# Performance work log

Measured on AMD Instinct MI355X. Metric: run time of the kernel, lower is better.

The kernel has to match this reference:

```python
import jax, jax.numpy as jnp
import numpy as np

HID = 256
IN_LSTM = 512
LAYER_NUM = 2


def _lstm_step(x, h, c, Wih, Whh, bih, bhh):
    # PyTorch LSTMCell: gates = x@Wih.T + bih + h@Whh.T + bhh, order i,f,g,o
    g = x @ Wih.T + bih + h @ Whh.T + bhh
    i, f, gg, o = jnp.split(g, 4, axis=-1)
    i = jax.nn.sigmoid(i); f = jax.nn.sigmoid(f)
    gg = jnp.tanh(gg); o = jax.nn.sigmoid(o)
    c2 = f * c + i * gg
    return o * jnp.tanh(c2), c2


def _run_direction(seq, Wih, Whh, bih, bhh, w_time, ts):
    # seq: [T, B, 512]; merge h/c via time_w_layer every ts steps;
    # at the merge step the *merged* h is written to the output buffer.
    T, B, _ = seq.shape
    chunks = seq.reshape(T // ts, ts, B, IN_LSTM)

    def chunk_fn(carry, xc):  # xc: [ts, B, 512]
        def step(hc, xt):
            h2, c2 = _lstm_step(xt, hc[0], hc[1], Wih, Whh, bih, bhh)
            return (h2, c2), (h2, c2)
        _, (hs, cs) = jax.lax.scan(step, carry, xc)  # hs: [ts, B, 256]
        hm = jnp.einsum('tbd,t->bd', hs, w_time)
        cm = jnp.einsum('tbd,t->bd', cs, w_time)
        return (hm, cm), hs.at[-1].set(hm)

    h0 = jnp.zeros((B, HID), seq.dtype)
    _, outs = jax.lax.scan(chunk_fn, (h0, h0), chunks)  # [T//ts, ts, B, 256]
    return outs.reshape(T, B, HID)


def setup_inputs() -> dict:
    key = jax.random.key(0)
    ks = jax.random.split(key, 16)
    B, T, D_IN, D_OUT, TS = 128, 1024, 128, 8, 8
    s_in = 1.0 / np.sqrt(D_IN)
    s_l = 1.0 / np.sqrt(HID)
    s_o = 1.0 / np.sqrt(2 * HID)
    return {
        'x': jax.random.normal(ks[0], (B, T, D_IN), jnp.float32),
        'W_in': jax.random.uniform(ks[1], (IN_LSTM, D_IN), jnp.float32, -s_in, s_in),
        'b_in': jax.random.uniform(ks[2], (IN_LSTM,), jnp.float32, -s_in, s_in),
        'Wih1': jax.random.uniform(ks[3], (4 * HID, IN_LSTM), jnp.float32, -s_l, s_l),
        'Whh1': jax.random.uniform(ks[4], (4 * HID, HID), jnp.float32, -s_l, s_l),
        'bih1': jax.random.uniform(ks[5], (4 * HID,), jnp.float32, -s_l, s_l),
        'bhh1': jax.random.uniform(ks[6], (4 * HID,), jnp.float32, -s_l, s_l),
        'Wih2': jax.random.uniform(ks[7], (4 * HID, IN_LSTM), jnp.float32, -s_l, s_l),
        'Whh2': jax.random.uniform(ks[8], (4 * HID, HID), jnp.float32, -s_l, s_l),
        'bih2': jax.random.uniform(ks[9], (4 * HID,), jnp.float32, -s_l, s_l),
        'bhh2': jax.random.uniform(ks[10], (4 * HID,), jnp.float32, -s_l, s_l),
        'w_time1': jax.random.uniform(ks[11], (TS,), jnp.float32, -1.0 / np.sqrt(TS), 1.0 / np.sqrt(TS)),
        'w_time2': jax.random.uniform(ks[12], (TS,), jnp.float32, -1.0 / np.sqrt(TS), 1.0 / np.sqrt(TS)),
        'W_out': jax.random.uniform(ks[13], (D_OUT, 2 * HID), jnp.float32, -s_o, s_o),
        'b_out': jax.random.uniform(ks[14], (D_OUT,), jnp.float32, -s_o, s_o),
        'batch_size': B,
        'time_steps': TS,
        'length': T,
        'r': 1,
    }


def reference(x, W_in, b_in, Wih1, Whh1, bih1, bhh1, Wih2, Whh2, bih2, bhh2,
              w_time1, w_time2, W_out, b_out, batch_size, time_steps, length, r):
    ts = int(time_steps)
    out = x @ W_in.T + b_in  # [B, T, 512]; dropout is identity in eval
    for _ in range(LAYER_NUM):
        seq = jnp.transpose(out, (1, 0, 2))  # [T, B, 512]
        o1 = _run_direction(seq, Wih1, Whh1, bih1, bhh1, w_time1, ts)
        # backward direction processes reversed input; outputs are stored in
        # processing order (NOT re-reversed), matching the original code.
        o2 = _run_direction(seq[::-1], Wih2, Whh2, bih2, bhh2, w_time2, ts)
        out = jnp.transpose(jnp.concatenate([o1, o2], axis=-1), (1, 0, 2))  # [B, T, 512]
    out = out @ W_out.T + b_out  # [B, T, output_dim]
    return jax.nn.log_softmax(out, axis=1)  # LogSoftmax(dim=1) over time, as in source
```

## Files before the change

### kernel.cpp

```cpp
#include <hip/hip_runtime.h>
#include <stdint.h>
#include <stddef.h>

#define HIDN 256
#define GATES 1024
#define INL 512
#define BB 128
#define TT 1024
#define TSS 8
#define DIN 128
#define DOUT 8

typedef unsigned short u16;
typedef unsigned int u32;
typedef unsigned long long u64;
typedef __bf16 bf16x8_t __attribute__((ext_vector_type(8)));
typedef float f32x4_t __attribute__((ext_vector_type(4)));
typedef short s16x8_t __attribute__((ext_vector_type(8)));
typedef u16 u16x4_t __attribute__((ext_vector_type(4)));

union V8 { s16x8_t s; bf16x8_t b; };
union U64x2 { u64 q[2]; s16x8_t s; };

#define MRK 0x0001000100010001ull

__device__ __forceinline__ u16 f2bf(float f){
  unsigned u = __builtin_bit_cast(unsigned, f);
  u += 0x7FFFu + ((u >> 16) & 1u);
  return (u16)(u >> 16);
}
__device__ __forceinline__ float bf2f(u16 h){
  unsigned u = ((unsigned)h) << 16;
  return __builtin_bit_cast(float, u);
}
__device__ __forceinline__ float sigmoidf_(float x){ return 1.f/(1.f + __expf(-x)); }
__device__ __forceinline__ float tanhf_(float x){
  float ax = fabsf(x);
  float e = __expf(-2.f*ax);
  float t = (1.f - e)/(1.f + e);
  return x < 0.f ? -t : t;
}

__global__ __launch_bounds__(256) void cvt_f32_bf16(const float* __restrict__ in,
                                                    u16* __restrict__ out, int n4){
  int i = blockIdx.x*256 + threadIdx.x;
  if (i < n4){
    float4 f = ((const float4*)in)[i];
    u16x4_t u;
    u[0] = f2bf(f.x); u[1] = f2bf(f.y); u[2] = f2bf(f.z); u[3] = f2bf(f.w);
    ((u16x4_t*)out)[i] = u;
  }
}

__global__ __launch_bounds__(256) void pack_whh(const float* __restrict__ Whh,
                                                u16* __restrict__ wf){
  int idx = blockIdx.x*256 + threadIdx.x;
  int l  = idx & 63;
  int kt = (idx >> 6) & 7;
  int nt = idx >> 9;
  int j = nt*16 + (l & 15);
  int k = kt*32 + (l >> 4)*8;
  const float* src = Whh + (long)j*HIDN + k;
  s16x8_t pk;
  #pragma unroll
  for (int e=0;e<8;e++) pk[e] = (short)f2bf(src[e]);
  *(s16x8_t*)(wf + (long)idx*8) = pk;
}

template<int XA, int OM>
__global__ __launch_bounds__(256, 2) void gemm_tile(
    const void* __restrict__ Av, const u16* __restrict__ W,
    u16* __restrict__ C,
    const float* __restrict__ bias1, const float* __restrict__ bias2,
    int K, int N, int srcT0, int sdir)
{
  __shared__ u16 As[128*32];
  __shared__ u16 Ws[128*32];
  const int tid = threadIdx.x;
  const int l = tid & 63, wid = tid >> 6;
  const int lr = l & 15, lg = l >> 4;
  const int wm = (wid >> 1)*64, wn = (wid & 1)*64;
  const int by = blockIdx.y, bx = blockIdx.x;
  const int n0 = bx*128;
  const int m0 = by*128;

  f32x4_t acc[4][4];
  #pragma unroll
  for (int i=0;i<4;i++)
    #pragma unroll
    for (int j=0;j<4;j++){ f32x4_t z = {0.f,0.f,0.f,0.f}; acc[i][j] = z; }

  const long abase = (long)(srcT0 + sdir*by)*128;
  const int srow = l >> 2;
  const int scol = (l & 3)*8;

  for (int k0 = 0; k0 < K; k0 += 32){
    __syncthreads();
    if (XA == 0){
      const u16* A = (const u16*)Av;
      #pragma unroll
      for (int c=0;c<2;c++){
        const int rb = wid*16 + c*64;
        __builtin_amdgcn_global_load_lds(
          (const __attribute__((address_space(1))) void*)
              (A + (abase + rb + srow)*(long)K + k0 + scol),
          (__attribute__((address_space(3))) void*)(&As[rb*32]),
          16, 0, 0);
      }
    } else {
      const float* A = (const float*)Av;
      const int xT = srcT0 + sdir*by;
      const int r0 = tid >> 2, c0 = (tid & 3)*8;
      #pragma unroll
      for (int c=0;c<2;c++){
        int row = r0 + c*64;
        const float* src = A + ((long)row*1024 + xT)*128 + k0 + c0;
        float4 f0 = *(const float4*)src;
        float4 f1 = *(const float4*)(src + 4);
        s16x8_t pk;
        pk[0]=(short)f2bf(f0.x); pk[1]=(short)f2bf(f0.y);
        pk[2]=(short)f2bf(f0.z); pk[3]=(short)f2bf(f0.w);
        pk[4]=(short)f2bf(f1.x); pk[5]=(short)f2bf(f1.y);
        pk[6]=(short)f2bf(f1.z); pk[7]=(short)f2bf(f1.w);
        *(s16x8_t*)(&As[row*32 + c0]) = pk;
      }
    }
    #pragma unroll
    for (int c=0;c<2;c++){
      const int rb = wid*16 + c*64;
      __builtin_amdgcn_global_load_lds(
        (const __attribute__((address_space(1))) void*)
            (W + (long)(n0 + rb + srow)*K + k0 + scol),
        (__attribute__((address_space(3))) void*)(&Ws[rb*32]),
        16, 0, 0);
    }
    __syncthreads();

    V8 af[4], bfr[4];
    #pragma unroll
    for (int i=0;i<4;i++)
      af[i].s = *(const s16x8_t*)(&As[(wm + i*16 + lr)*32 + lg*8]);
    #pragma unroll
    for (int j=0;j<4;j++)
      bfr[j].s = *(const s16x8_t*)(&Ws[(wn + j*16 + lr)*32 + lg*8]);
    #pragma unroll
    for (int i=0;i<4;i++)
      #pragma unroll
      for (int j=0;j<4;j++)
        acc[i][j] = __builtin_amdgcn_mfma_f32_16x16x32_bf16(af[i].b, bfr[j].b, acc[i][j], 0,0,0);
  }

  #pragma unroll
  for (int i=0;i<4;i++){
    #pragma unroll
    for (int j=0;j<4;j++){
      if (OM == 0){
        int col = n0 + wn + j*16 + lr;
        float bb = bias1 ? bias1[col] : 0.f;
        if (bias2) bb += bias2[col];
        #pragma unroll
        for (int r=0;r<4;r++){
          int mrow = m0 + wm + i*16 + lg*4 + r;
          C[(long)mrow*N + col] = f2bf(acc[i][j][r] + bb);
        }
      } else {
        int colb = n0 + wn + j*16;
        int col = colb + lr;
        int g   = colb >> 8;
        int hb2 = (colb >> 7) & 1;
        int w2  = (colb >> 4) & 7;
        int slice = (wm >> 4) + i;
        float bb = bias1[col] + bias2[col];
        u16x4_t v;
        #pragma unroll
        for (int r=0;r<4;r++) v[r] = f2bf(acc[i][j][r] + bb);
        long dst = ((((long)by*8 + slice)*2 + hb2)*8 + w2)*1024
                 + (long)l*16 + g*4;
        *(u16x4_t*)(C + dst) = v;
      }
    }
  }
}

__global__ __launch_bounds__(512, 2) void lstm_rec7(
    const u16* __restrict__ pre0, const u16* __restrict__ pre1,
    const u16* __restrict__ wf0, const u16* __restrict__ wf1,
    const float* __restrict__ wt0, const float* __restrict__ wt1,
    u16* __restrict__ out,
    int outBase, int CT, int isFirst,
    u16* __restrict__ hstate,
    float* __restrict__ cstate,
    u16* __restrict__ hx)
{
  const int bid = blockIdx.x;
  const int hb  = bid >> 4;
  const int p   = bid & 15;
  const int dir = p >> 3, slice = p & 7;
  const int tid = threadIdx.x;
  const int l = tid & 63, w = tid >> 6;
  const int lr = l & 15, lg = l >> 4;

  const u16*   wf  = dir ? wf1 : wf0;
  const float* wtg = dir ? wt1 : wt0;
  const u16*   pre = dir ? pre1 : pre0;

  V8 bwOwn[4][4], bwPeer[4][4];
  #pragma unroll
  for (int g=0; g<4; g++){
    const int nt = g*16 + hb*8 + w;
    const u16* base = wf + ((long)nt*8*64 + l)*8;
    const long ownOff  = (long)(hb*4)*64*8;
    const long peerOff = (long)((1-hb)*4)*64*8;
    #pragma unroll
    for (int j=0; j<4; j++){
      bwOwn [g][j].s = *(const s16x8_t*)(base + ownOff  + (long)j*64*8);
      bwPeer[g][j].s = *(const s16x8_t*)(base + peerOff + (long)j*64*8);
    }
  }

  __shared__ u16 h_buf[2][16][136];

  const int cr = tid >> 5, cc4 = (tid & 31)*4;
  u64 h0v = 0;
  if (!isFirst){
    const u16* src = hstate + dir*32768 + (slice*16 + cr)*256 + hb*128 + cc4;
    h0v = *(const u64*)src;
  }
  *(u64*)&h_buf[0][cr][cc4] = h0v;
  float c[4], hacc[4] = {0,0,0,0}, cacc[4] = {0,0,0,0};
  {
    const long cb = ((long)(dir*16 + slice*2 + hb)*512 + tid)*4;
    #pragma unroll
    for (int r=0;r<4;r++) c[r] = isFirst ? 0.f : cstate[cb + r];
  }
  float wreg[8];
  #pragma unroll
  for (int i=0;i<8;i++) wreg[i] = wtg[i];

  u16*       myx   = hx + (long)(p*2 + hb)*2*2048;
  const u16* peerx = hx + (long)(p*2 + (1-hb))*2*2048;

  __hip_atomic_store((u64*)(myx + cr*128 + cc4), h0v & ~MRK,
                     __ATOMIC_RELAXED, __HIP_MEMORY_SCOPE_AGENT);
  __syncthreads();

  const u16* preT = pre + (((long)slice*2 + hb)*8 + w)*1024 + (long)l*16;
  s16x8_t pfA = *(const s16x8_t*)(preT);
  s16x8_t pfB = *(const s16x8_t*)(preT + 8);

  for (int t = 0; t < CT; t++){
    f32x4_t acc[4];
    #pragma unroll
    for (int r=0; r<4; r++){
      acc[0][r] = bf2f((u16)pfA[r]);
      acc[1][r] = bf2f((u16)pfA[4+r]);
      acc[2][r] = bf2f((u16)pfB[r]);
      acc[3][r] = bf2f((u16)pfB[4+r]);
    }
    if (t + 1 < CT){
      const u16* pp = preT + (long)(t+1)*131072;
      pfA = *(const s16x8_t*)(pp);
      pfB = *(const s16x8_t*)(pp + 8);
    }

    const u64 exp = ((t>>1)&1) ? MRK : 0ull;
    const u64* qb = (const u64*)(peerx + (long)(t&1)*2048)
                  + (lr*32 + lg*2);
    u64 q[8];
    #pragma unroll
    for (int j=0;j<4;j++)
      #pragma unroll
      for (int k=0;k<2;k++)
        q[j*2+k] = __hip_atomic_load(qb + j*8 + k,
                      __ATOMIC_RELAXED, __HIP_MEMORY_SCOPE_AGENT);

    {
      V8 af[4];
      const u16* hb0 = &h_buf[t&1][lr][lg*8];
      #pragma unroll
      for (int j=0;j<4;j++)
        af[j].s = *(const s16x8_t*)(hb0 + j*32);
      #pragma unroll
      for (int g=0;g<4;g++)
        #pragma unroll
        for (int j=0;j<4;j++)
          acc[g] = __builtin_amdgcn_mfma_f32_16x16x32_bf16(
              af[j].b, bwOwn[g][j].b, acc[g], 0,0,0);
    }

    {
      int tries = 0;
      while (true){
        int ok = 1;
        #pragma unroll
        for (int i=0;i<8;i++) ok &= ((q[i] & MRK) == exp);
        if (__all(ok)) break;
        if (++tries > (1<<16)) break;
        __builtin_amdgcn_s_sleep(1);
        #pragma unroll
        for (int j=0;j<4;j++)
          #pragma unroll
          for (int k=0;k<2;k++)
            q[j*2+k] = __hip_atomic_load(qb + j*8 + k,
                          __ATOMIC_RELAXED, __HIP_MEMORY_SCOPE_AGENT);
      }
    }
    {
      V8 pafr[4];
      #pragma unroll
      for (int j=0;j<4;j++){
        U64x2 uq;
        uq.q[0] = q[j*2]; uq.q[1] = q[j*2+1];
        pafr[j].s = uq.s;
      }
      #pragma unroll
      for (int g=0;g<4;g++)
        #pragma unroll
        for (int j=0;j<4;j++)
          acc[g] = __builtin_amdgcn_mfma_f32_16x16x32_bf16(
              pafr[j].b, bwPeer[g][j].b, acc[g], 0,0,0);
    }

    const float wtv = wreg[t & 7];
    const bool last = (t & 7) == 7;
    float hout[4];
    #pragma unroll
    for (int r=0;r<4;r++){
      float iv = sigmoidf_(acc[0][r]);
      float fv = sigmoidf_(acc[1][r]);
      float gv = tanhf_  (acc[2][r]);
      float ov = sigmoidf_(acc[3][r]);
      float cn = fv*c[r] + iv*gv;
      float hh = ov*tanhf_(cn);
      float ha = hacc[r] + wtv*hh;
      float ca = cacc[r] + wtv*cn;
      hout[r] = last ? ha : hh;
      c[r]    = last ? ca : cn;
      hacc[r] = last ? 0.f : ha;
      cacc[r] = last ? 0.f : ca;
    }

    #pragma unroll
    for (int r=0;r<4;r++)
      h_buf[(t+1)&1][lg*4 + r][w*16 + lr] = f2bf(hout[r]);
    __syncthreads();

    if (t < CT - 1){
      const u64 pm = (((t+1)>>1)&1) ? MRK : 0ull;
      u64 v = *(const u64*)&h_buf[(t+1)&1][cr][cc4];
      v = (v & ~MRK) | pm;
      __hip_atomic_store((u64*)(myx + (long)((t+1)&1)*2048 + cr*128 + cc4), v,
                         __ATOMIC_RELAXED, __HIP_MEMORY_SCOPE_AGENT);
    }

    {
      u16x4_t v = *(const u16x4_t*)&h_buf[(t+1)&1][cr][cc4];
      const long orow = (long)(outBase + t)*128 + slice*16 + cr;
      *(u16x4_t*)(out + orow*512 + dir*256 + hb*128 + cc4) = v;
    }
  }

  {
    u16* dst = hstate + dir*32768 + (slice*16 + cr)*256 + hb*128 + cc4;
    *(u16x4_t*)dst = *(const u16x4_t*)&h_buf[CT&1][cr][cc4];
  }
  {
    const long cb = ((long)(dir*16 + slice*2 + hb)*512 + tid)*4;
    #pragma unroll
    for (int r=0;r<4;r++) cstate[cb + r] = c[r];
  }
}

__global__ __launch_bounds__(256) void kout(const u16* __restrict__ Ab,
    const u16* __restrict__ Wo, const float* __restrict__ bo,
    float* __restrict__ op, int chunkRow0)
{
  __shared__ u16 Ws[4096];
  __shared__ u16 Rs[32*520];
  const int tid = threadIdx.x;
  {
    int f = tid*8;
    *(s16x8_t*)&Ws[f] = *(const s16x8_t*)(Wo + f);
    *(s16x8_t*)&Ws[f+2048] = *(const s16x8_t*)(Wo + f + 2048);
  }
  const long row0 = (long)blockIdx.x*32;
  #pragma unroll
  for (int i=0;i<8;i++){
    int f = tid*8 + i*2048;
    int rr = f >> 9, cc = f & 511;
    *(s16x8_t*)&Rs[rr*520 + cc] = *(const s16x8_t*)(Ab + (row0+rr)*512 + cc);
  }
  __syncthreads();
  const int rr = tid >> 3, d = tid & 7;
  float s = bo[d];
  for (int k=0;k<512;k+=8){
    s16x8_t a = *(const s16x8_t*)&Rs[rr*520 + k];
    s16x8_t wv = *(const s16x8_t*)&Ws[d*512 + k];
    #pragma unroll
    for (int e=0;e<8;e++)
      s += bf2f((u16)a[e]) * bf2f((u16)wv[e]);
  }
  const long grow = chunkRow0 + row0 + rr;
  const int tt = (int)(grow >> 7), b2 = (int)(grow & 127);
  op[((long)b2*1024 + tt)*8 + d] = s;
}

__global__ __launch_bounds__(256) void lsm(float* __restrict__ io){
  const int b = blockIdx.x >> 3, d = blockIdx.x & 7;
  const int tid = threadIdx.x;
  __shared__ float red[4];
  float v[4];
  float mx = -3.4e38f;
  const long base = (long)b*1024*8 + d;
  #pragma unroll
  for (int i=0;i<4;i++){
    v[i] = io[base + (long)(tid + i*256)*8];
    mx = fmaxf(mx, v[i]);
  }
  #pragma unroll
  for (int off=32; off>=1; off>>=1) mx = fmaxf(mx, __shfl_down(mx, off, 64));
  if ((tid & 63) == 0) red[tid >> 6] = mx;
  __syncthreads();
  mx = fmaxf(fmaxf(red[0],red[1]), fmaxf(red[2],red[3]));
  __syncthreads();
  float s = 0.f;
  #pragma unroll
  for (int i=0;i<4;i++) s += __expf(v[i]-mx);
  #pragma unroll
  for (int off=32; off>=1; off>>=1) s += __shfl_down(s, off, 64);
  if ((tid & 63) == 0) red[tid >> 6] = s;
  __syncthreads();
  s = red[0]+red[1]+red[2]+red[3];
  float lse = mx + __logf(s);
  #pragma unroll
  for (int i=0;i<4;i++) io[base + (long)(tid + i*256)*8] = v[i] - lse;
}

extern "C" void kernel_launch(void* const* d_in, const int* in_sizes, int n_in,
                              void* d_out, int out_size, void* d_ws, size_t ws_size,
                              hipStream_t stream){
  const float* x     = (const float*)d_in[0];
  const float* W_in  = (const float*)d_in[1];
  const float* b_in  = (const float*)d_in[2];
  const float* Wih1  = (const float*)d_in[3];
  const float* Whh1  = (const float*)d_in[4];
  const float* bih1  = (const float*)d_in[5];
  const float* bhh1  = (const float*)d_in[6];
  const float* Wih2  = (const float*)d_in[7];
  const float* Whh2  = (const float*)d_in[8];
  const float* bih2  = (const float*)d_in[9];
  const float* bhh2  = (const float*)d_in[10];
  const float* wt1   = (const float*)d_in[11];
  const float* wt2   = (const float*)d_in[12];
  const float* W_out = (const float*)d_in[13];
  const float* b_out = (const float*)d_in[14];

  auto rnd = [](size_t b){ return (b + 255) & ~(size_t)255; };

  const size_t ACT1B   = (size_t)TT*BB*512*2;
  const size_t WIHB    = (size_t)GATES*INL*2;
  const size_t WFRAGB  = (size_t)GATES*HIDN*2;
  const size_t WINB    = (size_t)INL*DIN*2;
  const size_t WOUTB   = (size_t)DOUT*INL*2;
  const size_t HSTB    = (size_t)2*BB*HIDN*2;
  const size_t CSTB    = (size_t)32*512*4*4;
  const size_t HXB     = (size_t)32*2*2048*2;

  const size_t fixedB = rnd(ACT1B) + 2*rnd(WIHB) + 2*rnd(WFRAGB) + rnd(WINB)
                      + rnd(WOUTB) + rnd(HSTB) + rnd(CSTB) + rnd(HXB);

  int CT = 8;
  const int cands[8] = {1024,512,256,128,64,32,16,8};
  for (int ci = 0; ci < 8; ci++){
    int cand = cands[ci];
    size_t need = fixedB + rnd((size_t)cand*BB*512*2) + 2*rnd((size_t)cand*BB*GATES*2);
    if (need <= ws_size){ CT = cand; break; }
  }
  const int nc = TT / CT;

  char* ws = (char*)d_ws;
  size_t off = 0;
  auto alloc = [&](size_t bytes) -> void* {
    void* p = ws + off;
    off += rnd(bytes);
    return p;
  };

  u16*   act1    = (u16*)alloc(ACT1B);
  u16*   Wihb0   = (u16*)alloc(WIHB);
  u16*   Wihb1   = (u16*)alloc(WIHB);
  u16*   wfrag0  = (u16*)alloc(WFRAGB);
  u16*   wfrag1  = (u16*)alloc(WFRAGB);
  u16*   Winb    = (u16*)alloc(WINB);
  u16*   Woutb   = (u16*)alloc(WOUTB);
  u16*   hstate  = (u16*)alloc(HSTB);
  float* cstate  = (float*)alloc(CSTB);
  u16*   hx      = (u16*)alloc(HXB);
  u16*   actchunk= (u16*)alloc((size_t)CT*BB*512*2);
  u16*   pre0    = (u16*)alloc((size_t)CT*BB*GATES*2);
  u16*   pre1    = (u16*)alloc((size_t)CT*BB*GATES*2);

  hipMemsetAsync(hx, 0xFF, HXB, stream);

  cvt_f32_bf16<<<(GATES*INL/4 + 255)/256, 256, 0, stream>>>(Wih1, Wihb0, GATES*INL/4);
  cvt_f32_bf16<<<(GATES*INL/4 + 255)/256, 256, 0, stream>>>(Wih2, Wihb1, GATES*INL/4);
  cvt_f32_bf16<<<(INL*DIN/4 + 255)/256, 256, 0, stream>>>(W_in, Winb, INL*DIN/4);
  cvt_f32_bf16<<<(DOUT*INL/4 + 255)/256, 256, 0, stream>>>(W_out, Woutb, DOUT*INL/4);
  pack_whh<<<128, 256, 0, stream>>>(Whh1, wfrag0);
  pack_whh<<<128, 256, 0, stream>>>(Whh2, wfrag1);

  for (int c2 = 0; c2 < nc; c2++){
    gemm_tile<1,0><<<dim3(4, CT), 256, 0, stream>>>(x, Winb, actchunk,
        b_in, nullptr, DIN, 512, c2*CT, 1);
    gemm_tile<0,1><<<dim3(8, CT), 256, 0, stream>>>(actchunk, Wihb0, pre0,
        bih1, bhh1, INL, GATES, 0, 1);
    gemm_tile<1,0><<<dim3(4, CT), 256, 0, stream>>>(x, Winb, actchunk,
        b_in, nullptr, DIN, 512, 1023 - c2*CT, -1);
    gemm_tile<0,1><<<dim3(8, CT), 256, 0, stream>>>(actchunk, Wihb1, pre1,
        bih2, bhh2, INL, GATES, 0, 1);
    lstm_rec7<<<dim3(32), 512, 0, stream>>>(pre0, pre1, wfrag0, wfrag1,
        wt1, wt2, act1, c2*CT, CT, c2 == 0, hstate, cstate, hx);
  }

  for (int c2 = 0; c2 < nc; c2++){
    gemm_tile<0,1><<<dim3(8, CT), 256, 0, stream>>>(act1, Wihb0, pre0,
        bih1, bhh1, INL, GATES, c2*CT, 1);
    gemm_tile<0,1><<<dim3(8, CT), 256, 0, stream>>>(act1, Wihb1, pre1,
        bih2, bhh2, INL, GATES, 1023 - c2*CT, -1);
    lstm_rec7<<<dim3(32), 512, 0, stream>>>(pre0, pre1, wfrag0, wfrag1,
        wt1, wt2, actchunk, 0, CT, c2 == 0, hstate, cstate, hx);
    kout<<<CT*4, 256, 0, stream>>>(actchunk, Woutb, b_out,
        (float*)d_out, c2*CT*128);
  }

  lsm<<<BB*DOUT, 256, 0, stream>>>((float*)d_out);
}
```

Baseline: 8.580 ms.

## Merge paired LSTM recurrence blocks into one 1024-thread block, dropping cross-block spin sync

Each recurrence block previously covered half the hidden units and swapped h halves with its partner through global-memory atomics and spin-waits at every timestep. Now one 1024-thread block per (direction, batch slice) holds all 256 hidden units, keeps the full Whh fragment set in registers, and reads the whole h from shared memory, so per-step sync is just __syncthreads. The precomputed-gate layout is changed to match, and the hx exchange buffer and its memset are removed. The cost is half as many blocks (16) and twice the register weight load per thread, which could limit occupancy or cause spills.

After: 22.09 ms. 157% more time.

```diff
diff --git a/kernel.cpp b/kernel.cpp
--- a/kernel.cpp
+++ b/kernel.cpp
@@ -20,9 +20,6 @@
 typedef u16 u16x4_t __attribute__((ext_vector_type(4)));
 
 union V8 { s16x8_t s; bf16x8_t b; };
-union U64x2 { u64 q[2]; s16x8_t s; };
-
-#define MRK 0x0001000100010001ull
 
 __device__ __forceinline__ u16 f2bf(float f){
   unsigned u = __builtin_bit_cast(unsigned, f);
@@ -167,34 +164,30 @@
         int colb = n0 + wn + j*16;
         int col = colb + lr;
         int g   = colb >> 8;
-        int hb2 = (colb >> 7) & 1;
-        int w2  = (colb >> 4) & 7;
+        int w2  = (colb >> 4) & 15;
         int slice = (wm >> 4) + i;
         float bb = bias1[col] + bias2[col];
         u16x4_t v;
         #pragma unroll
         for (int r=0;r<4;r++) v[r] = f2bf(acc[i][j][r] + bb);
-        long dst = ((((long)by*8 + slice)*2 + hb2)*8 + w2)*1024
-                 + (long)l*16 + g*4;
+        long dst = (((long)by*8 + slice)*16 + w2)*1024
+                 + (long)(lg*16 + lr)*16 + g*4;
         *(u16x4_t*)(C + dst) = v;
       }
     }
   }
 }
 
-__global__ __launch_bounds__(512, 2) void lstm_rec7(
+__global__ __launch_bounds__(1024, 4) void lstm_rec9(
     const u16* __restrict__ pre0, const u16* __restrict__ pre1,
     const u16* __restrict__ wf0, const u16* __restrict__ wf1,
     const float* __restrict__ wt0, const float* __restrict__ wt1,
     u16* __restrict__ out,
     int outBase, int CT, int isFirst,
     u16* __restrict__ hstate,
-    float* __restrict__ cstate,
-    u16* __restrict__ hx)
+    float* __restrict__ cstate)
 {
-  const int bid = blockIdx.x;
-  const int hb  = bid >> 4;
-  const int p   = bid & 15;
+  const int p = blockIdx.x;
   const int dir = p >> 3, slice = p & 7;
   const int tid = threadIdx.x;
   const int l = tid & 63, w = tid >> 6;
@@ -204,32 +197,27 @@
   const float* wtg = dir ? wt1 : wt0;
   const u16*   pre = dir ? pre1 : pre0;
 
-  V8 bwOwn[4][4], bwPeer[4][4];
+  V8 bw[4][8];
   #pragma unroll
   for (int g=0; g<4; g++){
-    const int nt = g*16 + hb*8 + w;
+    const int nt = g*16 + w;
     const u16* base = wf + ((long)nt*8*64 + l)*8;
-    const long ownOff  = (long)(hb*4)*64*8;
-    const long peerOff = (long)((1-hb)*4)*64*8;
-    #pragma unroll
-    for (int j=0; j<4; j++){
-      bwOwn [g][j].s = *(const s16x8_t*)(base + ownOff  + (long)j*64*8);
-      bwPeer[g][j].s = *(const s16x8_t*)(base + peerOff + (long)j*64*8);
-    }
-  }
-
-  __shared__ u16 h_buf[2][16][136];
-
-  const int cr = tid >> 5, cc4 = (tid & 31)*4;
+    #pragma unroll
+    for (int kt=0; kt<8; kt++)
+      bw[g][kt].s = *(const s16x8_t*)(base + (long)kt*64*8);
+  }
+
+  __shared__ u16 h_buf[2][16][264];
+
+  const int cr = tid >> 6, cc4 = (tid & 63)*4;
   u64 h0v = 0;
-  if (!isFirst){
-    const u16* src = hstate + dir*32768 + (slice*16 + cr)*256 + hb*128 + cc4;
-    h0v = *(const u64*)src;
-  }
+  if (!isFirst)
+    h0v = *(const u64*)(hstate + dir*32768 + (slice*16 + cr)*256 + cc4);
   *(u64*)&h_buf[0][cr][cc4] = h0v;
+
   float c[4], hacc[4] = {0,0,0,0}, cacc[4] = {0,0,0,0};
   {
-    const long cb = ((long)(dir*16 + slice*2 + hb)*512 + tid)*4;
+    const long cb = ((long)p*1024 + tid)*4;
     #pragma unroll
     for (int r=0;r<4;r++) c[r] = isFirst ? 0.f : cstate[cb + r];
   }
@@ -237,14 +225,9 @@
   #pragma unroll
   for (int i=0;i<8;i++) wreg[i] = wtg[i];
 
-  u16*       myx   = hx + (long)(p*2 + hb)*2*2048;
-  const u16* peerx = hx + (long)(p*2 + (1-hb))*2*2048;
-
-  __hip_atomic_store((u64*)(myx + cr*128 + cc4), h0v & ~MRK,
-                     __ATOMIC_RELAXED, __HIP_MEMORY_SCOPE_AGENT);
   __syncthreads();
 
-  const u16* preT = pre + (((long)slice*2 + hb)*8 + w)*1024 + (long)l*16;
+  const u16* preT = pre + ((long)slice*16 + w)*1024 + (long)l*16;
   s16x8_t pfA = *(const s16x8_t*)(preT);
   s16x8_t pfB = *(const s16x8_t*)(preT + 8);
 
@@ -263,62 +246,14 @@
       pfB = *(const s16x8_t*)(pp + 8);
     }
 
-    const u64 exp = ((t>>1)&1) ? MRK : 0ull;
-    const u64* qb = (const u64*)(peerx + (long)(t&1)*2048)
-                  + (lr*32 + lg*2);
-    u64 q[8];
-    #pragma unroll
-    for (int j=0;j<4;j++)
+    #pragma unroll
+    for (int kt=0; kt<8; kt++){
+      V8 af;
+      af.s = *(const s16x8_t*)(&h_buf[t&1][lr][kt*32 + lg*8]);
       #pragma unroll
-      for (int k=0;k<2;k++)
-        q[j*2+k] = __hip_atomic_load(qb + j*8 + k,
-                      __ATOMIC_RELAXED, __HIP_MEMORY_SCOPE_AGENT);
-
-    {
-      V8 af[4];
-      const u16* hb0 = &h_buf[t&1][lr][lg*8];
-      #pragma unroll
-      for (int j=0;j<4;j++)
-        af[j].s = *(const s16x8_t*)(hb0 + j*32);
-      #pragma unroll
-      for (int g=0;g<4;g++)
-        #pragma unroll
-        for (int j=0;j<4;j++)
-          acc[g] = __builtin_amdgcn_mfma_f32_16x16x32_bf16(
-              af[j].b, bwOwn[g][j].b, acc[g], 0,0,0);
-    }
-
-    {
-      int tries = 0;
-      while (true){
-        int ok = 1;
-        #pragma unroll
-        for (int i=0;i<8;i++) ok &= ((q[i] & MRK) == exp);
-        if (__all(ok)) break;
-        if (++tries > (1<<16)) break;
-        __builtin_amdgcn_s_sleep(1);
-        #pragma unroll
-        for (int j=0;j<4;j++)
-          #pragma unroll
-          for (int k=0;k<2;k++)
-            q[j*2+k] = __hip_atomic_load(qb + j*8 + k,
-                          __ATOMIC_RELAXED, __HIP_MEMORY_SCOPE_AGENT);
-      }
-    }
-    {
-      V8 pafr[4];
-      #pragma unroll
-      for (int j=0;j<4;j++){
-        U64x2 uq;
-        uq.q[0] = q[j*2]; uq.q[1] = q[j*2+1];
-        pafr[j].s = uq.s;
-      }
-      #pragma unroll
-      for (int g=0;g<4;g++)
-        #pragma unroll
-        for (int j=0;j<4;j++)
-          acc[g] = __builtin_amdgcn_mfma_f32_16x16x32_bf16(
-              pafr[j].b, bwPeer[g][j].b, acc[g], 0,0,0);
+      for (int g=0; g<4; g++)
+        acc[g] = __builtin_amdgcn_mfma_f32_16x16x32_bf16(
+            af.b, bw[g][kt].b, acc[g], 0,0,0);
     }
 
     const float wtv = wreg[t & 7];
@@ -345,27 +280,17 @@
       h_buf[(t+1)&1][lg*4 + r][w*16 + lr] = f2bf(hout[r]);
     __syncthreads();
 
-    if (t < CT - 1){
-      const u64 pm = (((t+1)>>1)&1) ? MRK : 0ull;
+    {
       u64 v = *(const u64*)&h_buf[(t+1)&1][cr][cc4];
-      v = (v & ~MRK) | pm;
-      __hip_atomic_store((u64*)(myx + (long)((t+1)&1)*2048 + cr*128 + cc4), v,
-                         __ATOMIC_RELAXED, __HIP_MEMORY_SCOPE_AGENT);
-    }
-
-    {
-      u16x4_t v = *(const u16x4_t*)&h_buf[(t+1)&1][cr][cc4];
       const long orow = (long)(outBase + t)*128 + slice*16 + cr;
-      *(u16x4_t*)(out + orow*512 + dir*256 + hb*128 + cc4) = v;
-    }
-  }
-
+      *(u64*)(out + orow*512 + dir*256 + cc4) = v;
+    }
+  }
+
+  *(u64*)(hstate + dir*32768 + (slice*16 + cr)*256 + cc4)
+      = *(const u64*)&h_buf[CT&1][cr][cc4];
   {
-    u16* dst = hstate + dir*32768 + (slice*16 + cr)*256 + hb*128 + cc4;
-    *(u16x4_t*)dst = *(const u16x4_t*)&h_buf[CT&1][cr][cc4];
-  }
-  {
-    const long cb = ((long)(dir*16 + slice*2 + hb)*512 + tid)*4;
+    const long cb = ((long)p*1024 + tid)*4;
     #pragma unroll
     for (int r=0;r<4;r++) cstate[cb + r] = c[r];
   }
@@ -463,11 +388,10 @@
   const size_t WINB    = (size_t)INL*DIN*2;
   const size_t WOUTB   = (size_t)DOUT*INL*2;
   const size_t HSTB    = (size_t)2*BB*HIDN*2;
-  const size_t CSTB    = (size_t)32*512*4*4;
-  const size_t HXB     = (size_t)32*2*2048*2;
+  const size_t CSTB    = (size_t)16*1024*4*4;
 
   const size_t fixedB = rnd(ACT1B) + 2*rnd(WIHB) + 2*rnd(WFRAGB) + rnd(WINB)
-                      + rnd(WOUTB) + rnd(HSTB) + rnd(CSTB) + rnd(HXB);
+                      + rnd(WOUTB) + rnd(HSTB) + rnd(CSTB);
 
   int CT = 8;
   const int cands[8] = {1024,512,256,128,64,32,16,8};
@@ -495,12 +419,9 @@
   u16*   Woutb   = (u16*)alloc(WOUTB);
   u16*   hstate  = (u16*)alloc(HSTB);
   float* cstate  = (float*)alloc(CSTB);
-  u16*   hx      = (u16*)alloc(HXB);
   u16*   actchunk= (u16*)alloc((size_t)CT*BB*512*2);
   u16*   pre0    = (u16*)alloc((size_t)CT*BB*GATES*2);
   u16*   pre1    = (u16*)alloc((size_t)CT*BB*GATES*2);
-
-  hipMemsetAsync(hx, 0xFF, HXB, stream);
 
   cvt_f32_bf16<<<(GATES*INL/4 + 255)/256, 256, 0, stream>>>(Wih1, Wihb0, GATES*INL/4);
   cvt_f32_bf16<<<(GATES*INL/4 + 255)/256, 256, 0, stream>>>(Wih2, Wihb1, GATES*INL/4);
@@ -518,8 +439,8 @@
         b_in, nullptr, DIN, 512, 1023 - c2*CT, -1);
     gemm_tile<0,1><<<dim3(8, CT), 256, 0, stream>>>(actchunk, Wihb1, pre1,
         bih2, bhh2, INL, GATES, 0, 1);
-    lstm_rec7<<<dim3(32), 512, 0, stream>>>(pre0, pre1, wfrag0, wfrag1,
-        wt1, wt2, act1, c2*CT, CT, c2 == 0, hstate, cstate, hx);
+    lstm_rec9<<<dim3(16), 1024, 0, stream>>>(pre0, pre1, wfrag0, wfrag1,
+        wt1, wt2, act1, c2*CT, CT, c2 == 0, hstate, cstate);
   }
 
   for (int c2 = 0; c2 < nc; c2++){
@@ -527,8 +448,8 @@
         bih1, bhh1, INL, GATES, c2*CT, 1);
     gemm_tile<0,1><<<dim3(8, CT), 256, 0, stream>>>(act1, Wihb1, pre1,
         bih2, bhh2, INL, GATES, 1023 - c2*CT, -1);
-    lstm_rec7<<<dim3(32), 512, 0, stream>>>(pre0, pre1, wfrag0, wfrag1,
-        wt1, wt2, actchunk, 0, CT, c2 == 0, hstate, cstate, hx);
+    lstm_rec9<<<dim3(16), 1024, 0, stream>>>(pre0, pre1, wfrag0, wfrag1,
+        wt1, wt2, actchunk, 0, CT, c2 == 0, hstate, cstate);
     kout<<<CT*4, 256, 0, stream>>>(actchunk, Woutb, b_out,
         (float*)d_out, c2*CT*128);
   }
```
